# Kernel optimization log

Hardware: AMD Instinct MI355X
Metric: run time of the kernel (lower is better)

## Reference

```python
import jax, jax.numpy as jnp
import numpy as np

# ShapeNet category -> contiguous segment range (16 categories, 50 segments)
SEG_LENS = np.array([4, 2, 2, 4, 4, 3, 3, 2, 4, 2, 6, 2, 3, 3, 3, 3], dtype=np.int32)
SHIFTS = np.concatenate([[0], np.cumsum(SEG_LENS)[:-1]]).astype(np.int32)
NUM_CAT = 16
IN_F = 256
MAX_SEG_COUNT = 6   # max len(seg) over categories
MAX_SEG = 49        # max segment id
N_PTS = 32768
BN_EPS = 1e-5


def setup_inputs() -> dict:
    key = jax.random.key(0)
    k1, k2, k3, k4 = jax.random.split(key, 4)
    features = jax.random.normal(k1, (N_PTS, IN_F), dtype=jnp.float32)
    W1 = jax.random.normal(k2, (IN_F, NUM_CAT * IN_F), dtype=jnp.float32) * (1.0 / np.sqrt(IN_F))
    gamma = jnp.ones((NUM_CAT * IN_F,), dtype=jnp.float32)
    beta = jnp.zeros((NUM_CAT * IN_F,), dtype=jnp.float32)
    Wc = jax.random.normal(k3, (NUM_CAT, IN_F, MAX_SEG_COUNT), dtype=jnp.float32) * (1.0 / np.sqrt(IN_F))
    bias = jnp.zeros((MAX_SEG_COUNT,), dtype=jnp.float32)
    cats = jax.random.randint(k4, (N_PTS,), 0, NUM_CAT, dtype=jnp.int32)
    return {
        "features": features, "W1": W1, "gamma": gamma, "beta": beta,
        "Wc": Wc, "bias": bias, "cats": cats,
        "shifts": jnp.asarray(SHIFTS), "seg_lens": jnp.asarray(SEG_LENS),
    }


def reference(features, W1, gamma, beta, Wc, bias, cats, shifts, seg_lens):
    N, F = features.shape
    C, _, S = Wc.shape
    # channel_rasing: Linear(bias=False) -> BatchNorm1d (batch stats) -> LeakyReLU(0.2)
    x = features @ W1                              # [N, C*F]
    mu = x.mean(axis=0)
    var = x.var(axis=0)                            # biased, as BatchNorm
    x = (x - mu) * jax.lax.rsqrt(var + BN_EPS) * gamma + beta
    x = jnp.where(x >= 0, x, 0.2 * x)              # LeakyReLU(0.2); Dropout = identity (eval)
    # UnaryConv: per-category matmul + shared bias -> [C, N, S]
    x = x.reshape(N, C, F)
    feats = jnp.einsum('ncf,cfs->cns', x, Wc) + bias
    # gather the assigned category's logits per point -> [N, S]
    logits = feats[cats, jnp.arange(N)]
    lsm = jax.nn.log_softmax(logits, axis=-1)
    # scatter (expressed as gather) into per-category segment ranges -> [N, MAX_SEG+1]
    sh = shifts[cats]                              # [N]
    ln = seg_lens[cats]                            # [N]
    k = jnp.arange(MAX_SEG + 1, dtype=jnp.int32)   # [50]
    j = k[None, :] - sh[:, None]                   # [N, 50]
    valid = (j >= 0) & (j < ln[:, None])
    jc = jnp.clip(j, 0, S - 1)
    out = jnp.where(valid, jnp.take_along_axis(lsm, jc, axis=1), 0.0)
    return out
```

## Files before the change

kernel.cpp:

```cpp
#include <hip/hip_runtime.h>
#include <hip/hip_bf16.h>
#include <math.h>

#define N_PTS 32768
#define IN_F  256
#define NUM_CAT 16
#define CF    4096
#define NSEG  6
#define OUTK  50
#define BN_EPS 1e-5f

typedef unsigned short u16;
typedef __attribute__((ext_vector_type(8))) short bf16x8;
typedef __attribute__((ext_vector_type(4))) float f32x4;
typedef __attribute__((ext_vector_type(8))) unsigned short u16x8;

#define OFF_G     0u
#define OFF_FBAR  65536u
#define OFF_SCALE 65792u
#define OFF_SHIFT 69888u
#define OFF_INT   73984u
#define OFF_FB    106832u
#define OFF_FBT   4301136u
#define OFF_W1T   8495440u
#define OFF_GP    9019728u
#define IO_COUNTS 0
#define IO_CATOFF 16
#define IO_TILEST 33
#define IO_NTILES 50
#define IO_CURSOR 51
#define IO_ORDER  67

__device__ __forceinline__ void gload_lds16(const void* g, void* l) {
    __builtin_amdgcn_global_load_lds(
        (const __attribute__((address_space(1))) void*)g,
        (__attribute__((address_space(3))) void*)l,
        16, 0, 0);
}
__device__ __forceinline__ u16 f2bf(float f) {
    unsigned int u = __float_as_uint(f);
    return (u16)((u + 0x7FFF + ((u >> 16) & 1)) >> 16);
}
__device__ __forceinline__ float bf2f(u16 h) {
    return __uint_as_float((unsigned int)h << 16);
}

__global__ __launch_bounds__(256) void k0_cvt(const float* __restrict__ F,
                                              u16* __restrict__ Fb,
                                              u16* __restrict__ FbT) {
    const int pb = blockIdx.x >> 2, fb = blockIdx.x & 3;
    const int p0 = pb * 64, f0 = fb * 64;
    const int tid = threadIdx.x;
    __shared__ u16 T[64][72];
    {
        int p = tid >> 2, fq = tid & 3;
        const float* src = &F[(size_t)(p0 + p) * IN_F + f0 + fq * 16];
        u16x8 o0, o1;
        float4 v0 = *(const float4*)&src[0];
        float4 v1 = *(const float4*)&src[4];
        float4 v2 = *(const float4*)&src[8];
        float4 v3 = *(const float4*)&src[12];
        o0[0]=f2bf(v0.x); o0[1]=f2bf(v0.y); o0[2]=f2bf(v0.z); o0[3]=f2bf(v0.w);
        o0[4]=f2bf(v1.x); o0[5]=f2bf(v1.y); o0[6]=f2bf(v1.z); o0[7]=f2bf(v1.w);
        o1[0]=f2bf(v2.x); o1[1]=f2bf(v2.y); o1[2]=f2bf(v2.z); o1[3]=f2bf(v2.w);
        o1[4]=f2bf(v3.x); o1[5]=f2bf(v3.y); o1[6]=f2bf(v3.z); o1[7]=f2bf(v3.w);
        u16* dst = &Fb[(size_t)(p0 + p) * IN_F + f0 + fq * 16];
        *(u16x8*)dst = o0; *(u16x8*)&dst[8] = o1;
        *(u16x8*)&T[p][fq * 16] = o0; *(u16x8*)&T[p][fq * 16 + 8] = o1;
    }
    __syncthreads();
    {
        int f = tid >> 2, pq = tid & 3;
        u16x8 a0, a1;
#pragma unroll
        for (int m = 0; m < 8; m++) { a0[m] = T[pq*16 + m][f]; a1[m] = T[pq*16 + 8 + m][f]; }
        u16* dst = &FbT[(size_t)(f0 + f) * N_PTS + p0 + pq * 16];
        *(u16x8*)dst = a0; *(u16x8*)&dst[8] = a1;
    }
}

__global__ __launch_bounds__(256) void k0b_w1t(const float* __restrict__ W1,
                                               u16* __restrict__ W1T) {
    __shared__ u16 T[64][65];
    const int kb = blockIdx.x & 3, jb = blockIdx.x >> 2;
    const int tid = threadIdx.x;
    {
        int kk = tid >> 2, j4 = (tid & 3) * 16;
        const float* src = &W1[(size_t)(kb * 64 + kk) * CF + jb * 64 + j4];
#pragma unroll
        for (int q = 0; q < 4; q++) {
            float4 v = *(const float4*)&src[q * 4];
            T[kk][j4 + q * 4 + 0] = f2bf(v.x); T[kk][j4 + q * 4 + 1] = f2bf(v.y);
            T[kk][j4 + q * 4 + 2] = f2bf(v.z); T[kk][j4 + q * 4 + 3] = f2bf(v.w);
        }
    }
    __syncthreads();
    {
        int jj = tid >> 2, ks = (tid & 3) * 16;
        int c = jb >> 2, n = (jb & 3) * 64 + jj;
        u16* dst = &W1T[((size_t)(c * 256 + n)) * 256 + kb * 64 + ks];
        u16x8 o0, o1;
#pragma unroll
        for (int m = 0; m < 8; m++) { o0[m] = T[ks + m][jj]; o1[m] = T[ks + 8 + m][jj]; }
        *(u16x8*)dst = o0;
        *(u16x8*)&dst[8] = o1;
    }
}

__global__ __launch_bounds__(256) void k1_gram(const u16* __restrict__ FbT,
                                               float* __restrict__ ws,
                                               int nchunk, int Kc) {
    const int TI[10] = {0,0,0,0,1,1,1,2,2,3};
    const int TJ[10] = {0,1,2,3,1,2,3,2,3,3};
    const int t = blockIdx.x % 10, chunk = blockIdx.x / 10;
    const int i0 = TI[t] * 64, j0 = TJ[t] * 64;
    const int r0 = chunk * Kc;
    const int tid = threadIdx.x;
    const int wv = tid >> 6, ln = tid & 63, g = ln >> 4, r16 = ln & 15;
    __shared__ __align__(16) u16 SA[2][4096];
    __shared__ __align__(16) u16 SB[2][4096];

    const int q0 = wv * 2, q1 = wv * 2 + 1;
    const int u_a = ((q0 * 64 + ln) & 7), row_a = (q0 * 64 + ln) >> 3;
    const int u_b = ((q1 * 64 + ln) & 7), row_b = (q1 * 64 + ln) >> 3;
    const int ka = ((u_a ^ (row_a & 7)) << 3), kb2 = ((u_b ^ (row_b & 7)) << 3);

    f32x4 acc[4];
#pragma unroll
    for (int nt = 0; nt < 4; nt++)
#pragma unroll
        for (int i = 0; i < 4; i++) acc[nt][i] = 0.f;

    const int nslab = Kc >> 6;
#define K1_STAGE(s, b)                                                              \
    {   int p0s = r0 + (s) * 64;                                                    \
        gload_lds16(FbT + (size_t)(i0 + row_a) * N_PTS + p0s + ka,                  \
                    (char*)SA[b] + q0 * 1024);                                      \
        gload_lds16(FbT + (size_t)(i0 + row_b) * N_PTS + p0s + kb2,                 \
                    (char*)SA[b] + q1 * 1024);                                      \
        gload_lds16(FbT + (size_t)(j0 + row_a) * N_PTS + p0s + ka,                  \
                    (char*)SB[b] + q0 * 1024);                                      \
        gload_lds16(FbT + (size_t)(j0 + row_b) * N_PTS + p0s + kb2,                 \
                    (char*)SB[b] + q1 * 1024);                                      \
    }

    K1_STAGE(0, 0);
    __syncthreads();
    for (int s = 0; s < nslab; s++) {
        const int b = s & 1;
        if (s + 1 < nslab) K1_STAGE(s + 1, b ^ 1);
#pragma unroll
        for (int ks = 0; ks < 2; ks++) {
            int ph = (ks * 4 + g) ^ (r16 & 7);
            bf16x8 a = *(const bf16x8*)((const char*)SA[b] + (wv * 16 + r16) * 128 + ph * 16);
#pragma unroll
            for (int nt = 0; nt < 4; nt++) {
                int nB = nt * 16 + r16;
                bf16x8 bb = *(const bf16x8*)((const char*)SB[b] + nB * 128 + ph * 16);
                acc[nt] = __builtin_amdgcn_mfma_f32_16x16x32_bf16(a, bb, acc[nt], 0, 0, 0);
            }
        }
        __syncthreads();
    }
    float* Gp = ws + OFF_GP + (size_t)chunk * 40960 + t * 4096;
#pragma unroll
    for (int nt = 0; nt < 4; nt++)
#pragma unroll
        for (int i = 0; i < 4; i++) {
            int row = wv * 16 + g * 4 + i, col = nt * 16 + r16;
            Gp[row * 64 + col] = acc[nt][i];
        }
}

__global__ __launch_bounds__(256) void k1b_colsum(const u16* __restrict__ FbT,
                                                  float* __restrict__ ws) {
    const int row = blockIdx.x, tid = threadIdx.x;
    const u16* r = FbT + (size_t)row * N_PTS;
    float s = 0.f;
    for (int i = tid * 8; i < N_PTS; i += 2048) {
        u16x8 v = *(const u16x8*)&r[i];
#pragma unroll
        for (int m = 0; m < 8; m++) s += bf2f(v[m]);
    }
#pragma unroll
    for (int off = 32; off >= 1; off >>= 1) s += __shfl_xor(s, off);
    __shared__ float ps[4];
    if ((tid & 63) == 0) ps[tid >> 6] = s;
    __syncthreads();
    if (tid == 0) ws[OFF_FBAR + row] = (ps[0] + ps[1] + ps[2] + ps[3]) * (1.0f / N_PTS);
    if (blockIdx.x == 0 && tid < 16) ((int*)(ws + OFF_INT))[IO_COUNTS + tid] = 0;
}

__global__ __launch_bounds__(256) void k2a_reduce(float* __restrict__ ws, int nchunk) {
    const int TI[10] = {0,0,0,0,1,1,1,2,2,3};
    const int TJ[10] = {0,1,2,3,1,2,3,2,3,3};
    const int e = blockIdx.x * 256 + threadIdx.x;
    const float* p = ws + OFF_GP + e;
    float s = 0.f;
#pragma unroll 8
    for (int c = 0; c < nchunk; c++) s += p[(size_t)c * 40960];
    int t = e >> 12, x = (e >> 6) & 63, y = e & 63;
    int a = TI[t] * 64 + x, b = TJ[t] * 64 + y;
    ws[OFF_G + a * 256 + b] = s;
    ws[OFF_G + b * 256 + a] = s;
}

__global__ __launch_bounds__(256) void k2b_stats(const float* __restrict__ W1,
                                                 const float* __restrict__ gamma,
                                                 const float* __restrict__ beta,
                                                 float* __restrict__ ws) {
    const int tid = threadIdx.x;
    const int j0 = blockIdx.x * 16;
    __shared__ __align__(16) float wl[16][256];
    __shared__ float pw[16][8];
#pragma unroll
    for (int q = 0; q < 4; q++) {
        float4 v = *(const float4*)&W1[(size_t)tid * CF + j0 + q * 4];
        wl[q * 4 + 0][tid] = v.x; wl[q * 4 + 1][tid] = v.y;
        wl[q * 4 + 2][tid] = v.z; wl[q * 4 + 3][tid] = v.w;
    }
    __syncthreads();
    float acc[16];
#pragma unroll
    for (int jj = 0; jj < 16; jj++) acc[jj] = 0.f;
    const float* G = ws + OFF_G;
    for (int b = 0; b < 256; b++) {
        float g = G[b * 256 + tid];
#pragma unroll
        for (int jj = 0; jj < 16; jj++) acc[jj] += g * wl[jj][b];
    }
    float fb = ws[OFF_FBAR + tid];
    const int lane = tid & 63, wave = tid >> 6;
#pragma unroll
    for (int jj = 0; jj < 16; jj++) {
        float v = wl[jj][tid] * acc[jj];
        float m = fb * wl[jj][tid];
#pragma unroll
        for (int off = 32; off >= 1; off >>= 1) {
            v += __shfl_xor(v, off);
            m += __shfl_xor(m, off);
        }
        if (lane == 0) { pw[jj][wave * 2] = v; pw[jj][wave * 2 + 1] = m; }
    }
    __syncthreads();
    if (tid < 16) {
        int jj = tid;
        float v = 0.f, m = 0.f;
        for (int w2 = 0; w2 < 4; w2++) { v += pw[jj][w2 * 2]; m += pw[jj][w2 * 2 + 1]; }
        float mu  = m;
        float var = v * (1.0f / N_PTS) - mu * mu;
        float sc  = gamma[j0 + jj] * rsqrtf(var + BN_EPS);
        float sh  = beta[j0 + jj] - mu * sc;
        ws[OFF_SCALE + j0 + jj] = sc;
        ws[OFF_SHIFT + j0 + jj] = sh;
    }
}

__global__ __launch_bounds__(256) void k3_hist(const int* __restrict__ cats,
                                               float* __restrict__ ws) {
    __shared__ int h[16];
    int tid = threadIdx.x;
    if (tid < 16) h[tid] = 0;
    __syncthreads();
    for (int n = blockIdx.x * 256 + tid; n < N_PTS; n += 64 * 256)
        atomicAdd(&h[cats[n]], 1);
    __syncthreads();
    int* wi = (int*)(ws + OFF_INT);
    if (tid < 16) atomicAdd(&wi[IO_COUNTS + tid], h[tid]);
}

__global__ void k4_prefix(float* __restrict__ ws) {
    int* wi = (int*)(ws + OFF_INT);
    if (threadIdx.x == 0) {
        int co = 0, ts = 0;
        wi[IO_CATOFF] = 0; wi[IO_TILEST] = 0;
        for (int c = 0; c < 16; c++) {
            int cnt = wi[IO_COUNTS + c];
            wi[IO_CURSOR + c] = co;
            co += cnt; ts += (cnt + 63) >> 6;
            wi[IO_CATOFF + c + 1] = co;
            wi[IO_TILEST + c + 1] = ts;
        }
        wi[IO_NTILES] = ts;
    }
}

__global__ __launch_bounds__(256) void k4b_scatter(const int* __restrict__ cats,
                                                   float* __restrict__ ws) {
    int* wi = (int*)(ws + OFF_INT);
    __shared__ int lh[16], lbase[16];
    const int tid = threadIdx.x;
    const int n0 = blockIdx.x * 512;
    if (tid < 16) lh[tid] = 0;
    __syncthreads();
    const int cA = cats[n0 + tid];
    const int cB = cats[n0 + 256 + tid];
    atomicAdd(&lh[cA], 1);
    atomicAdd(&lh[cB], 1);
    __syncthreads();
    if (tid < 16) lbase[tid] = atomicAdd(&wi[IO_CURSOR + tid], lh[tid]);
    __syncthreads();
    if (tid < 16) lh[tid] = 0;
    __syncthreads();
    int rA = atomicAdd(&lh[cA], 1);
    wi[IO_ORDER + lbase[cA] + rA] = n0 + tid;
    int rB = atomicAdd(&lh[cB], 1);
    wi[IO_ORDER + lbase[cB] + rB] = n0 + 256 + tid;
}

__global__ __launch_bounds__(256) void k5_mfma(const u16* __restrict__ Fb,
                                               const u16* __restrict__ W1T,
                                               const float* __restrict__ Wc,
                                               const float* __restrict__ bias,
                                               const int* __restrict__ shifts,
                                               const int* __restrict__ seg_lens,
                                               const float* __restrict__ ws,
                                               float* __restrict__ out) {
    const int* wi = (const int*)(ws + OFF_INT);
    const int t = blockIdx.x;
    if (t >= wi[IO_NTILES]) return;
    int c = 0;
    while (!(t >= wi[IO_TILEST + c] && t < wi[IO_TILEST + c + 1])) c++;
    const int lt = t - wi[IO_TILEST + c];
    const int base = wi[IO_CATOFF + c] + lt * 64;
    const int npts = min(64, wi[IO_COUNTS + c] - lt * 64);
    const int tid = threadIdx.x;
    const int wv = tid >> 6, ln = tid & 63;
    const int g = ln >> 4, r16 = ln & 15;

    __shared__ __align__(16) unsigned char U[65536];
    __shared__ float scl[256], shl[256], wcl[1536];
    __shared__ int plds[64];

    if (tid < 64) plds[tid] = wi[IO_ORDER + base + min(tid, npts - 1)];
    scl[tid] = ws[OFF_SCALE + c * 256 + tid];
    shl[tid] = ws[OFF_SHIFT + c * 256 + tid];
#pragma unroll
    for (int i = 0; i < 6; i++) wcl[tid + i * 256] = Wc[(size_t)c * 1536 + tid + i * 256];
    __syncthreads();

    const u16* W1Tc = W1T + (size_t)c * 65536;

#pragma unroll
    for (int s = 0; s < 8; s++) {
        int flat = s * 256 + tid;
        int pt = flat >> 5, u = flat & 31;
        const u16* src = Fb + (size_t)plds[pt] * 256 + ((u ^ (pt & 7)) << 3);
        gload_lds16(src, U + (size_t)(s * 4 + wv) * 1024);
    }
#pragma unroll
    for (int rr = 0; rr < 4; rr++) {
        int n = wv * 64 + rr * 16 + (ln >> 2);
        int q = ln & 3;
        const u16* src = W1Tc + (size_t)n * 256 + 0 + ((q ^ (n & 3)) << 3);
        gload_lds16(src, U + 32768 + (size_t)(wv * 64 + rr * 16) * 64);
    }
    __syncthreads();

    f32x4 acc[4][4];
#pragma unroll
    for (int mt = 0; mt < 4; mt++)
#pragma unroll
        for (int nt = 0; nt < 4; nt++)
#pragma unroll
            for (int i = 0; i < 4; i++) acc[mt][nt][i] = 0.f;

    int cur = 0;
    for (int kc = 0; kc < 8; kc++) {
        if (kc < 7) {
            int k0 = (kc + 1) * 32;
#pragma unroll
            for (int rr = 0; rr < 4; rr++) {
                int n = wv * 64 + rr * 16 + (ln >> 2);
                int q = ln & 3;
                const u16* src = W1Tc + (size_t)n * 256 + k0 + ((q ^ (n & 3)) << 3);
                gload_lds16(src, U + 32768 + (size_t)(cur ^ 1) * 16384
                                 + (size_t)(wv * 64 + rr * 16) * 64);
            }
        }
        bf16x8 af[4], bf[4];
#pragma unroll
        for (int mt = 0; mt < 4; mt++) {
            int row = mt * 16 + r16;
            int phys = (kc * 4 + g) ^ (row & 7);
            af[mt] = *(const bf16x8*)(U + (size_t)row * 512 + phys * 16);
        }
#pragma unroll
        for (int nt = 0; nt < 4; nt++) {
            int n = wv * 64 + nt * 16 + r16;
            int phys = g ^ (n & 3);
            bf[nt] = *(const bf16x8*)(U + 32768 + (size_t)cur * 16384
                                      + (size_t)n * 64 + phys * 16);
        }
#pragma unroll
        for (int mt = 0; mt < 4; mt++)
#pragma unroll
            for (int nt = 0; nt < 4; nt++)
                acc[mt][nt] = __builtin_amdgcn_mfma_f32_16x16x32_bf16(
                    af[mt], bf[nt], acc[mt][nt], 0, 0, 0);
        __syncthreads();
        cur ^= 1;
    }

    u16* X = (u16*)U;
#pragma unroll
    for (int mt = 0; mt < 4; mt++)
#pragma unroll
        for (int nt = 0; nt < 4; nt++) {
            int col = wv * 64 + nt * 16 + r16;
            float sc = scl[col], sh = shl[col];
#pragma unroll
            for (int i = 0; i < 4; i++) {
                int pt = mt * 16 + g * 4 + i;
                float x = acc[mt][nt][i] * sc + sh;
                x = (x >= 0.f) ? x : 0.2f * x;
                X[pt * 272 + col] = f2bf(x);
            }
        }
    __syncthreads();

    const int tm = tid & 15, tn = tid >> 4;
    float pl[4][6];
#pragma unroll
    for (int i = 0; i < 4; i++)
#pragma unroll
        for (int s = 0; s < 6; s++) pl[i][s] = 0.f;
#pragma unroll
    for (int j = 0; j < 16; j++) {
        int n = tn * 16 + j;
#pragma unroll
        for (int i = 0; i < 4; i++) {
            float x = bf2f(X[(tm * 4 + i) * 272 + n]);
#pragma unroll
            for (int s = 0; s < 6; s++) pl[i][s] += x * wcl[n * 6 + s];
        }
    }
    float* red = (float*)(U + 36864);
#pragma unroll
    for (int i = 0; i < 4; i++)
#pragma unroll
        for (int s = 0; s < 6; s++)
            red[(tn * 64 + tm * 4 + i) * 6 + s] = pl[i][s];
    __syncthreads();

    if (tid < 64 && tid < npts) {
        const int m = tid;
        float lg[6];
#pragma unroll
        for (int s = 0; s < 6; s++) lg[s] = bias[s];
        for (int w = 0; w < 16; w++)
#pragma unroll
            for (int s = 0; s < 6; s++) lg[s] += red[(w * 64 + m) * 6 + s];
        float mx = lg[0];
#pragma unroll
        for (int s = 1; s < 6; s++) mx = fmaxf(mx, lg[s]);
        float se = 0.f;
#pragma unroll
        for (int s = 0; s < 6; s++) se += expf(lg[s] - mx);
        float lse = mx + logf(se);
        const int pid = plds[m];
        const int sh = shifts[c], ln2 = seg_lens[c];
        float* orow = out + (size_t)pid * OUTK;
        for (int k = 0; k < OUTK; k++) {
            int j = k - sh;
            orow[k] = (j >= 0 && j < ln2) ? (lg[j] - lse) : 0.f;
        }
    }
}

extern "C" void kernel_launch(void* const* d_in, const int* in_sizes, int n_in,
                              void* d_out, int out_size, void* d_ws, size_t ws_size,
                              hipStream_t stream) {
    const float* F      = (const float*)d_in[0];
    const float* W1     = (const float*)d_in[1];
    const float* gamma  = (const float*)d_in[2];
    const float* beta   = (const float*)d_in[3];
    const float* Wc     = (const float*)d_in[4];
    const float* bias   = (const float*)d_in[5];
    const int*  cats    = (const int*)d_in[6];
    const int*  shifts  = (const int*)d_in[7];
    const int*  seglens = (const int*)d_in[8];
    float* out = (float*)d_out;
    float* ws  = (float*)d_ws;
    u16* Fb  = (u16*)(ws + OFF_FB);
    u16* FbT = (u16*)(ws + OFF_FBT);
    u16* W1T = (u16*)(ws + OFF_W1T);

    int nchunk = 64;
    if (ws_size < ((size_t)OFF_GP + 40960ull * 64) * 4) nchunk = 32;
    if (ws_size < ((size_t)OFF_GP + 40960ull * 32) * 4) nchunk = 16;
    const int Kc = N_PTS / nchunk;

    hipLaunchKernelGGL(k0_cvt,      dim3(2048), dim3(256), 0, stream, F, Fb, FbT);
    hipLaunchKernelGGL(k0b_w1t,     dim3(256),  dim3(256), 0, stream, W1, W1T);
    hipLaunchKernelGGL(k1_gram,     dim3(10 * nchunk), dim3(256), 0, stream, FbT, ws, nchunk, Kc);
    hipLaunchKernelGGL(k1b_colsum,  dim3(256),  dim3(256), 0, stream, FbT, ws);
    hipLaunchKernelGGL(k2a_reduce,  dim3(160),  dim3(256), 0, stream, ws, nchunk);
    hipLaunchKernelGGL(k2b_stats,   dim3(256),  dim3(256), 0, stream, W1, gamma, beta, ws);
    hipLaunchKernelGGL(k3_hist,     dim3(64),   dim3(256), 0, stream, cats, ws);
    hipLaunchKernelGGL(k4_prefix,   dim3(1),    dim3(64),  0, stream, ws);
    hipLaunchKernelGGL(k4b_scatter, dim3(64),   dim3(256), 0, stream, cats, ws);
    hipLaunchKernelGGL(k5_mfma,     dim3(528),  dim3(256), 0, stream,
                       Fb, W1T, Wc, bias, shifts, seglens, ws, out);
}
```

Measured before the change: 122.7 us.

## Load W1 fragments directly to registers and fuse BN/classifier epilogue with shuffles

```diff
diff --git a/kernel.cpp b/kernel.cpp
--- a/kernel.cpp
+++ b/kernel.cpp
@@ -328,7 +328,7 @@
     const int wv = tid >> 6, ln = tid & 63;
     const int g = ln >> 4, r16 = ln & 15;
 
-    __shared__ __align__(16) unsigned char U[65536];
+    __shared__ __align__(16) unsigned char U[32768];
     __shared__ float scl[256], shl[256], wcl[1536];
     __shared__ int plds[64];
 
@@ -338,8 +338,6 @@
 #pragma unroll
     for (int i = 0; i < 6; i++) wcl[tid + i * 256] = Wc[(size_t)c * 1536 + tid + i * 256];
     __syncthreads();
-
-    const u16* W1Tc = W1T + (size_t)c * 65536;
 
 #pragma unroll
     for (int s = 0; s < 8; s++) {
@@ -348,14 +346,13 @@
         const u16* src = Fb + (size_t)plds[pt] * 256 + ((u ^ (pt & 7)) << 3);
         gload_lds16(src, U + (size_t)(s * 4 + wv) * 1024);
     }
-#pragma unroll
-    for (int rr = 0; rr < 4; rr++) {
-        int n = wv * 64 + rr * 16 + (ln >> 2);
-        int q = ln & 3;
-        const u16* src = W1Tc + (size_t)n * 256 + 0 + ((q ^ (n & 3)) << 3);
-        gload_lds16(src, U + 32768 + (size_t)(wv * 64 + rr * 16) * 64);
-    }
-    __syncthreads();
+    __syncthreads();
+
+    const u16* W1Tc = W1T + (size_t)c * 65536;
+    const u16* wp0 = W1Tc + (size_t)(wv * 64 +  0 + r16) * 256 + g * 8;
+    const u16* wp1 = W1Tc + (size_t)(wv * 64 + 16 + r16) * 256 + g * 8;
+    const u16* wp2 = W1Tc + (size_t)(wv * 64 + 32 + r16) * 256 + g * 8;
+    const u16* wp3 = W1Tc + (size_t)(wv * 64 + 48 + r16) * 256 + g * 8;
 
     f32x4 acc[4][4];
 #pragma unroll
@@ -365,20 +362,21 @@
 #pragma unroll
             for (int i = 0; i < 4; i++) acc[mt][nt][i] = 0.f;
 
-    int cur = 0;
+    bf16x8 bf[2][4];
+    bf[0][0] = *(const bf16x8*)(wp0);
+    bf[0][1] = *(const bf16x8*)(wp1);
+    bf[0][2] = *(const bf16x8*)(wp2);
+    bf[0][3] = *(const bf16x8*)(wp3);
+
+#pragma unroll
     for (int kc = 0; kc < 8; kc++) {
         if (kc < 7) {
-            int k0 = (kc + 1) * 32;
-#pragma unroll
-            for (int rr = 0; rr < 4; rr++) {
-                int n = wv * 64 + rr * 16 + (ln >> 2);
-                int q = ln & 3;
-                const u16* src = W1Tc + (size_t)n * 256 + k0 + ((q ^ (n & 3)) << 3);
-                gload_lds16(src, U + 32768 + (size_t)(cur ^ 1) * 16384
-                                 + (size_t)(wv * 64 + rr * 16) * 64);
-            }
-        }
-        bf16x8 af[4], bf[4];
+            bf[(kc + 1) & 1][0] = *(const bf16x8*)(wp0 + (kc + 1) * 32);
+            bf[(kc + 1) & 1][1] = *(const bf16x8*)(wp1 + (kc + 1) * 32);
+            bf[(kc + 1) & 1][2] = *(const bf16x8*)(wp2 + (kc + 1) * 32);
+            bf[(kc + 1) & 1][3] = *(const bf16x8*)(wp3 + (kc + 1) * 32);
+        }
+        bf16x8 af[4];
 #pragma unroll
         for (int mt = 0; mt < 4; mt++) {
             int row = mt * 16 + r16;
@@ -386,71 +384,51 @@
             af[mt] = *(const bf16x8*)(U + (size_t)row * 512 + phys * 16);
         }
 #pragma unroll
-        for (int nt = 0; nt < 4; nt++) {
-            int n = wv * 64 + nt * 16 + r16;
-            int phys = g ^ (n & 3);
-            bf[nt] = *(const bf16x8*)(U + 32768 + (size_t)cur * 16384
-                                      + (size_t)n * 64 + phys * 16);
-        }
-#pragma unroll
         for (int mt = 0; mt < 4; mt++)
 #pragma unroll
             for (int nt = 0; nt < 4; nt++)
                 acc[mt][nt] = __builtin_amdgcn_mfma_f32_16x16x32_bf16(
-                    af[mt], bf[nt], acc[mt][nt], 0, 0, 0);
-        __syncthreads();
-        cur ^= 1;
-    }
-
-    u16* X = (u16*)U;
+                    af[mt], bf[kc & 1][nt], acc[mt][nt], 0, 0, 0);
+    }
+
+    __syncthreads();
+    float* red2 = (float*)U;
 #pragma unroll
     for (int mt = 0; mt < 4; mt++)
 #pragma unroll
-        for (int nt = 0; nt < 4; nt++) {
-            int col = wv * 64 + nt * 16 + r16;
-            float sc = scl[col], sh = shl[col];
-#pragma unroll
-            for (int i = 0; i < 4; i++) {
+        for (int i = 0; i < 4; i++) {
+            float pl[6] = {0.f, 0.f, 0.f, 0.f, 0.f, 0.f};
+#pragma unroll
+            for (int nt = 0; nt < 4; nt++) {
+                int col = wv * 64 + nt * 16 + r16;
+                float x = acc[mt][nt][i] * scl[col] + shl[col];
+                x = (x >= 0.f) ? x : 0.2f * x;
+#pragma unroll
+                for (int s = 0; s < 6; s++) pl[s] += x * wcl[col * 6 + s];
+            }
+#pragma unroll
+            for (int s = 0; s < 6; s++) {
+                pl[s] += __shfl_xor(pl[s], 1);
+                pl[s] += __shfl_xor(pl[s], 2);
+                pl[s] += __shfl_xor(pl[s], 4);
+                pl[s] += __shfl_xor(pl[s], 8);
+            }
+            if (r16 == 0) {
                 int pt = mt * 16 + g * 4 + i;
-                float x = acc[mt][nt][i] * sc + sh;
-                x = (x >= 0.f) ? x : 0.2f * x;
-                X[pt * 272 + col] = f2bf(x);
+#pragma unroll
+                for (int s = 0; s < 6; s++) red2[(pt * 4 + wv) * 6 + s] = pl[s];
             }
         }
     __syncthreads();
 
-    const int tm = tid & 15, tn = tid >> 4;
-    float pl[4][6];
-#pragma unroll
-    for (int i = 0; i < 4; i++)
-#pragma unroll
-        for (int s = 0; s < 6; s++) pl[i][s] = 0.f;
-#pragma unroll
-    for (int j = 0; j < 16; j++) {
-        int n = tn * 16 + j;
-#pragma unroll
-        for (int i = 0; i < 4; i++) {
-            float x = bf2f(X[(tm * 4 + i) * 272 + n]);
-#pragma unroll
-            for (int s = 0; s < 6; s++) pl[i][s] += x * wcl[n * 6 + s];
-        }
-    }
-    float* red = (float*)(U + 36864);
-#pragma unroll
-    for (int i = 0; i < 4; i++)
-#pragma unroll
-        for (int s = 0; s < 6; s++)
-            red[(tn * 64 + tm * 4 + i) * 6 + s] = pl[i][s];
-    __syncthreads();
-
     if (tid < 64 && tid < npts) {
-        const int m = tid;
         float lg[6];
 #pragma unroll
         for (int s = 0; s < 6; s++) lg[s] = bias[s];
-        for (int w = 0; w < 16; w++)
-#pragma unroll
-            for (int s = 0; s < 6; s++) lg[s] += red[(w * 64 + m) * 6 + s];
+#pragma unroll
+        for (int w = 0; w < 4; w++)
+#pragma unroll
+            for (int s = 0; s < 6; s++) lg[s] += red2[(tid * 4 + w) * 6 + s];
         float mx = lg[0];
 #pragma unroll
         for (int s = 1; s < 6; s++) mx = fmaxf(mx, lg[s]);
@@ -458,7 +436,7 @@
 #pragma unroll
         for (int s = 0; s < 6; s++) se += expf(lg[s] - mx);
         float lse = mx + logf(se);
-        const int pid = plds[m];
+        const int pid = plds[tid];
         const int sh = shifts[c], ln2 = seg_lens[c];
         float* orow = out + (size_t)pid * OUTK;
         for (int k = 0; k < OUTK; k++) {
```

Result: faster. 115.3 us (-6.0%).
